# Optimization experiments

Measured on AMD Instinct MI355X. Metric: run time of the kernel, lower is better.

Reference implementation:

```python
import jax, jax.numpy as jnp
import numpy as np

N, F, E = 2048, 512, 32  # batch, n_features (attention length), embedding_dim


def setup_inputs() -> dict:
    key = jax.random.key(0)
    ks = jax.random.split(key, 8)
    xav = np.sqrt(2.0 / (F + E))  # xavier_normal std for [F, E] params
    X = jax.random.normal(ks[0], (N, F), dtype=jnp.float32)
    Xi = jax.random.randint(ks[1], (N,), 0, 2).astype(jnp.float32)
    idx = jax.random.randint(ks[2], (N,), 0, F)
    I = jax.nn.one_hot(idx, F, dtype=jnp.float32)  # one-hot feature selector
    S = (jax.random.uniform(ks[3], (N, F)) < 0.5).astype(jnp.float32)
    S = S.at[:, 0].set(1.0)  # guarantee non-empty context per row
    return {
        "X": X, "Xi": Xi, "I": I, "S": S,
        "xi_w": jax.random.normal(ks[4], (F, E), jnp.float32) * xav,
        "xi_b": jax.random.normal(ks[5], (F, E), jnp.float32) * xav,
        "xs_w": jax.random.normal(ks[6], (F, E), jnp.float32) * xav,
        "xs_b": jax.random.normal(ks[7], (F, E), jnp.float32) * xav,
    }


def stable_softmax(x):
    # softmax along last dim; rows that are entirely -inf produce zeros
    m = jnp.max(x, axis=-1, keepdims=True)
    m = jnp.where(jnp.isfinite(m), m, jnp.zeros_like(m))
    e = jnp.exp(x - m)
    s = jnp.sum(e, axis=-1, keepdims=True)
    return e / jnp.maximum(s, jnp.asarray(1e-9, x.dtype))


def reference(X, Xi, I, S, xi_w, xi_b, xs_w, xs_b):
    # --- map_xs (attention aggregator) ---
    # FX: [N, F, E]; note the original reuses xs_featurizer_bias for the I-term
    FX = X[:, :, None] * xs_w[None] + xs_b[None] + (I @ xs_b)[:, None, :]
    keep = (S[:, :, None] * S[:, None, :]) > 0  # [N, F, F]
    mask = jnp.where(keep, 0.0, -jnp.inf).astype(FX.dtype)
    scale = jnp.asarray(1.0 / np.sqrt(E), FX.dtype)
    scores = mask + jnp.einsum('nqe,nke->nqk', FX * scale, FX)
    attn = stable_softmax(scores)  # [N, F, F]
    Fxs = jnp.einsum('nqk,nke->nqe', attn, FX).sum(axis=1) / S.sum(axis=1)[:, None]  # [N, E]
    # --- map_xi ---
    Iw = I @ xi_w  # [N, E]
    Ib = I @ xi_b  # [N, E]
    Fxi = Xi[:, None] * Iw + Ib
    # --- score / logz / logprob (binary, exp score) ---
    ulogp = jnp.log(jnp.exp(jnp.sum(Fxi * Fxs, axis=-1)))
    s0 = jnp.exp(jnp.sum(Ib * Fxs, axis=-1))          # Xi = 0
    s1 = jnp.exp(jnp.sum((Iw + Ib) * Fxs, axis=-1))   # Xi = 1
    logz = jnp.log(s0 + s1)
    return ulogp - logz  # [N]
```

## Files before the change

kernel.cpp:

```cpp
#include <hip/hip_runtime.h>
#include <math.h>

#define FF 512
#define EE 32
#define RS 40
#define FCAP 416
#define NTCAP 26

typedef __attribute__((ext_vector_type(8))) short bf16x8;
typedef __attribute__((ext_vector_type(4))) float f32x4;

#define SFOLD 0.5050092f

__device__ __forceinline__ unsigned short f2bf(float x) {
    unsigned int u = __float_as_uint(x);
    return (unsigned short)((u + 0x7fffu + ((u >> 16) & 1u)) >> 16);
}

__device__ __forceinline__ void zh4(f32x4 d, float4 g, float& z, float& h) {
    float e0 = __builtin_amdgcn_exp2f(d[0]);
    float e1 = __builtin_amdgcn_exp2f(d[1]);
    float e2 = __builtin_amdgcn_exp2f(d[2]);
    float e3 = __builtin_amdgcn_exp2f(d[3]);
    z += (e0 + e1) + (e2 + e3);
    h = fmaf(e0, g.x, fmaf(e1, g.y, fmaf(e2, g.z, fmaf(e3, g.w, h))));
}

template <int NC>
__device__ __forceinline__ void fused_cols(const unsigned short* __restrict__ myrow,
                                           const float* __restrict__ gs,
                                           float* __restrict__ a_sh,
                                           int c0, int nt, int cnt, float pad,
                                           int lane, int grp) {
    bf16x8 bf[NC];
#pragma unroll
    for (int c = 0; c < NC; ++c)
        bf[c] = *(const bf16x8*)(myrow + (size_t)(c0 + c) * 16 * RS);
    float zA[NC], zB[NC], hA[NC], hB[NC];
#pragma unroll
    for (int c = 0; c < NC; ++c) { zA[c] = 0.f; zB[c] = 0.f; hA[c] = 0.f; hB[c] = 0.f; }
    const unsigned short* ap = myrow;
    const float* gp = gs + grp * 4;
    int i = 0;
    for (; i + 2 <= nt; i += 2) {
        bf16x8 a0 = *(const bf16x8*)(ap);
        bf16x8 a1 = *(const bf16x8*)(ap + 16 * RS);
        ap += 32 * RS;
        float4 g0 = *(const float4*)(gp);
        float4 g1 = *(const float4*)(gp + 16);
        gp += 32;
#pragma unroll
        for (int c = 0; c < NC; ++c) {
            f32x4 d0 = {0.f, 0.f, 0.f, 0.f};
            f32x4 d1 = {0.f, 0.f, 0.f, 0.f};
            d0 = __builtin_amdgcn_mfma_f32_16x16x32_bf16(a0, bf[c], d0, 0, 0, 0);
            d1 = __builtin_amdgcn_mfma_f32_16x16x32_bf16(a1, bf[c], d1, 0, 0, 0);
            zh4(d0, g0, zA[c], hA[c]);
            zh4(d1, g1, zB[c], hB[c]);
        }
    }
    if (i < nt) {
        bf16x8 a0 = *(const bf16x8*)(ap);
        float4 g0 = *(const float4*)(gp);
#pragma unroll
        for (int c = 0; c < NC; ++c) {
            f32x4 d0 = {0.f, 0.f, 0.f, 0.f};
            d0 = __builtin_amdgcn_mfma_f32_16x16x32_bf16(a0, bf[c], d0, 0, 0, 0);
            zh4(d0, g0, zA[c], hA[c]);
        }
    }
#pragma unroll
    for (int c = 0; c < NC; ++c) {
        float z = zA[c] + zB[c];
        float h = hA[c] + hB[c];
        z += __shfl_xor(z, 16); z += __shfl_xor(z, 32);
        h += __shfl_xor(h, 16); h += __shfl_xor(h, 32);
        int q = (c0 + c) * 16 + lane;
        float val = (lane < 16 && q < cnt) ? h / fmaxf(z - pad, 1e-9f) : 0.f;
        val += __shfl_xor(val, 1);
        val += __shfl_xor(val, 2);
        val += __shfl_xor(val, 4);
        val += __shfl_xor(val, 8);
        if (lane == 0) atomicAdd(a_sh, val);
    }
}

extern "C" __global__ void __launch_bounds__(512, 8)
model_kernel(const float* __restrict__ X, const float* __restrict__ Xi,
             const float* __restrict__ I, const float* __restrict__ S,
             const float* __restrict__ xi_w, const float* __restrict__ xi_b,
             const float* __restrict__ xs_w, const float* __restrict__ xs_b,
             float* __restrict__ out) {
    const int n = blockIdx.x;
    const int tid = threadIdx.x;
    const int lane = tid & 63;
    const int wv = tid >> 6;
    const int l15 = lane & 15;
    const int grp = lane >> 4;

    __shared__ __align__(16) unsigned short fxb[FCAP * RS];
    __shared__ unsigned short lst[FF];
    __shared__ __align__(16) float gs[FCAP];
    __shared__ __align__(16) float idxb[EE];
    __shared__ __align__(16) float iw_sh[EE];
    __shared__ float a_sh;
    __shared__ int sh_idx;
    __shared__ int wbase[8];

    const float* Srow = S + (size_t)n * FF;
    const float* Irow = I + (size_t)n * FF;
    const float* Xrow = X + (size_t)n * FF;

    if (Irow[tid] > 0.5f) sh_idx = tid;
    bool act = Srow[tid] > 0.f;
    unsigned long long m = __ballot(act);
    int nb = __popcll(m & ((1ull << lane) - 1ull));
    if (lane == 0) wbase[wv] = __popcll(m);
    __syncthreads();

    int off = 0;
    for (int i = 0; i < wv; ++i) off += wbase[i];
    if (act) lst[off + nb] = (unsigned short)tid;
    int cntr = 0;
#pragma unroll
    for (int i = 0; i < 8; ++i) cntr += wbase[i];
    const int cnt = (cntr < FCAP) ? cntr : FCAP;
    int nt0 = (cnt + 15) >> 4;
    const int nt = (nt0 < NTCAP) ? nt0 : NTCAP;
    const int ntp16 = nt * 16;
    const int jend = ((nt + 1) >> 1) * 32;
    const int idx = sh_idx;
    if (tid < EE) {
        idxb[tid] = xs_b[idx * EE + tid];
        iw_sh[tid] = xi_w[idx * EE + tid];
    }
    if (tid == 0) a_sh = 0.f;
    __syncthreads();

    for (int jb = 0; jb < jend; jb += 64) {
        int j = jb + (tid >> 3);
        int e4 = (tid & 7) * 4;
        float part = 0.f;
        if (j < jend) {
            unsigned short h0 = 0, h1 = 0, h2 = 0, h3 = 0;
            if (j < cnt) {
                int f = lst[j];
                float xv = Xrow[f];
                float4 w4 = *(const float4*)(xs_w + f * EE + e4);
                float4 b4 = *(const float4*)(xs_b + f * EE + e4);
                float4 i4 = *(const float4*)(idxb + e4);
                float r0 = SFOLD * fmaf(xv, w4.x, b4.x + i4.x);
                float r1 = SFOLD * fmaf(xv, w4.y, b4.y + i4.y);
                float r2 = SFOLD * fmaf(xv, w4.z, b4.z + i4.z);
                float r3 = SFOLD * fmaf(xv, w4.w, b4.w + i4.w);
                h0 = f2bf(r0); h1 = f2bf(r1); h2 = f2bf(r2); h3 = f2bf(r3);
                const float* iw = iw_sh + e4;
                part = fmaf(r0, iw[0], fmaf(r1, iw[1], fmaf(r2, iw[2], r3 * iw[3])));
            }
            ushort4 pk = make_ushort4(h0, h1, h2, h3);
            *(ushort4*)(fxb + j * RS + e4) = pk;
        }
        part += __shfl_xor(part, 1);
        part += __shfl_xor(part, 2);
        part += __shfl_xor(part, 4);
        if ((tid & 7) == 0 && j < jend) gs[j] = part;
    }
    __syncthreads();

    const unsigned short* myrow = fxb + (size_t)l15 * RS + grp * 8;
    const float pad = (float)(ntp16 - cnt);

    const int cbase = nt >> 3, crem = nt & 7;
    const int ncols = cbase + (wv < crem ? 1 : 0);
    const int c0 = wv * cbase + (wv < crem ? wv : crem);

    switch (ncols) {
        case 1: fused_cols<1>(myrow, gs, &a_sh, c0, nt, cnt, pad, lane, grp); break;
        case 2: fused_cols<2>(myrow, gs, &a_sh, c0, nt, cnt, pad, lane, grp); break;
        case 3: fused_cols<3>(myrow, gs, &a_sh, c0, nt, cnt, pad, lane, grp); break;
        case 4: fused_cols<2>(myrow, gs, &a_sh, c0, nt, cnt, pad, lane, grp);
                fused_cols<2>(myrow, gs, &a_sh, c0 + 2, nt, cnt, pad, lane, grp); break;
        default: break;
    }
    __syncthreads();

    if (tid == 0) {
        float a = a_sh / ((float)cnt * SFOLD);
        float xiv = Xi[n];
        float mm = fmaxf(a, 0.f);
        float sp = mm + logf(__expf(a - mm) + __expf(-mm));
        out[n] = xiv * a - sp;
    }
}

extern "C" void kernel_launch(void* const* d_in, const int* in_sizes, int n_in,
                              void* d_out, int out_size, void* d_ws, size_t ws_size,
                              hipStream_t stream) {
    const float* X    = (const float*)d_in[0];
    const float* Xi   = (const float*)d_in[1];
    const float* I    = (const float*)d_in[2];
    const float* S    = (const float*)d_in[3];
    const float* xi_w = (const float*)d_in[4];
    const float* xi_b = (const float*)d_in[5];
    const float* xs_w = (const float*)d_in[6];
    const float* xs_b = (const float*)d_in[7];
    float* out = (float*)d_out;
    const int N = in_sizes[1];
    hipLaunchKernelGGL(model_kernel, dim3(N), dim3(512), 0, stream,
                       X, Xi, I, S, xi_w, xi_b, xs_w, xs_b, out);
}
```

Measured before the change: 102.4 us.

## Split attention work across column groups and key halves with shared partial sums

Reorganizes the fused score/softmax loop so waves are arranged as 4 column groups times 2 key-range halves, each processing more query columns per loaded key tile. Partial softmax denominators and numerators are accumulated per query into shared arrays via atomics, then normalized and reduced in a final pass. This aims to increase A-operand reuse and balance work across waves, at the cost of shared atomics, an extra barrier, and losing dual independent accumulators.

```diff
diff --git a/kernel.cpp b/kernel.cpp
--- a/kernel.cpp
+++ b/kernel.cpp
@@ -27,22 +27,21 @@
 }
 
 template <int NC>
-__device__ __forceinline__ void fused_cols(const unsigned short* __restrict__ myrow,
-                                           const float* __restrict__ gs,
-                                           float* __restrict__ a_sh,
-                                           int c0, int nt, int cnt, float pad,
-                                           int lane, int grp) {
+__device__ __forceinline__ void fused(const unsigned short* __restrict__ myrow,
+                                      const float* __restrict__ gs,
+                                      float* __restrict__ Zp, float* __restrict__ Hp,
+                                      int c0, int s_lo, int s_hi, int lane, int grp) {
     bf16x8 bf[NC];
 #pragma unroll
     for (int c = 0; c < NC; ++c)
         bf[c] = *(const bf16x8*)(myrow + (size_t)(c0 + c) * 16 * RS);
-    float zA[NC], zB[NC], hA[NC], hB[NC];
-#pragma unroll
-    for (int c = 0; c < NC; ++c) { zA[c] = 0.f; zB[c] = 0.f; hA[c] = 0.f; hB[c] = 0.f; }
-    const unsigned short* ap = myrow;
-    const float* gp = gs + grp * 4;
-    int i = 0;
-    for (; i + 2 <= nt; i += 2) {
+    float z[NC], h[NC];
+#pragma unroll
+    for (int c = 0; c < NC; ++c) { z[c] = 0.f; h[c] = 0.f; }
+    const unsigned short* ap = myrow + (size_t)s_lo * 16 * RS;
+    const float* gp = gs + s_lo * 16 + grp * 4;
+    int s = s_lo;
+    for (; s + 2 <= s_hi; s += 2) {
         bf16x8 a0 = *(const bf16x8*)(ap);
         bf16x8 a1 = *(const bf16x8*)(ap + 16 * RS);
         ap += 32 * RS;
@@ -55,33 +54,29 @@
             f32x4 d1 = {0.f, 0.f, 0.f, 0.f};
             d0 = __builtin_amdgcn_mfma_f32_16x16x32_bf16(a0, bf[c], d0, 0, 0, 0);
             d1 = __builtin_amdgcn_mfma_f32_16x16x32_bf16(a1, bf[c], d1, 0, 0, 0);
-            zh4(d0, g0, zA[c], hA[c]);
-            zh4(d1, g1, zB[c], hB[c]);
-        }
-    }
-    if (i < nt) {
+            zh4(d0, g0, z[c], h[c]);
+            zh4(d1, g1, z[c], h[c]);
+        }
+    }
+    if (s < s_hi) {
         bf16x8 a0 = *(const bf16x8*)(ap);
         float4 g0 = *(const float4*)(gp);
 #pragma unroll
         for (int c = 0; c < NC; ++c) {
             f32x4 d0 = {0.f, 0.f, 0.f, 0.f};
             d0 = __builtin_amdgcn_mfma_f32_16x16x32_bf16(a0, bf[c], d0, 0, 0, 0);
-            zh4(d0, g0, zA[c], hA[c]);
+            zh4(d0, g0, z[c], h[c]);
         }
     }
 #pragma unroll
     for (int c = 0; c < NC; ++c) {
-        float z = zA[c] + zB[c];
-        float h = hA[c] + hB[c];
-        z += __shfl_xor(z, 16); z += __shfl_xor(z, 32);
-        h += __shfl_xor(h, 16); h += __shfl_xor(h, 32);
-        int q = (c0 + c) * 16 + lane;
-        float val = (lane < 16 && q < cnt) ? h / fmaxf(z - pad, 1e-9f) : 0.f;
-        val += __shfl_xor(val, 1);
-        val += __shfl_xor(val, 2);
-        val += __shfl_xor(val, 4);
-        val += __shfl_xor(val, 8);
-        if (lane == 0) atomicAdd(a_sh, val);
+        float zz = z[c], hh = h[c];
+        zz += __shfl_xor(zz, 16); zz += __shfl_xor(zz, 32);
+        hh += __shfl_xor(hh, 16); hh += __shfl_xor(hh, 32);
+        if (lane < 16) {
+            atomicAdd(&Zp[(c0 + c) * 16 + lane], zz);
+            atomicAdd(&Hp[(c0 + c) * 16 + lane], hh);
+        }
     }
 }
 
@@ -101,6 +96,8 @@
     __shared__ __align__(16) unsigned short fxb[FCAP * RS];
     __shared__ unsigned short lst[FF];
     __shared__ __align__(16) float gs[FCAP];
+    __shared__ __align__(16) float Zp[FCAP];
+    __shared__ __align__(16) float Hp[FCAP];
     __shared__ __align__(16) float idxb[EE];
     __shared__ __align__(16) float iw_sh[EE];
     __shared__ float a_sh;
@@ -112,6 +109,8 @@
     const float* Xrow = X + (size_t)n * FF;
 
     if (Irow[tid] > 0.5f) sh_idx = tid;
+    if (tid < FCAP) { Zp[tid] = 0.f; Hp[tid] = 0.f; }
+    if (tid == 0) a_sh = 0.f;
     bool act = Srow[tid] > 0.f;
     unsigned long long m = __ballot(act);
     int nb = __popcll(m & ((1ull << lane) - 1ull));
@@ -128,20 +127,18 @@
     int nt0 = (cnt + 15) >> 4;
     const int nt = (nt0 < NTCAP) ? nt0 : NTCAP;
     const int ntp16 = nt * 16;
-    const int jend = ((nt + 1) >> 1) * 32;
     const int idx = sh_idx;
     if (tid < EE) {
         idxb[tid] = xs_b[idx * EE + tid];
         iw_sh[tid] = xi_w[idx * EE + tid];
     }
-    if (tid == 0) a_sh = 0.f;
-    __syncthreads();
-
-    for (int jb = 0; jb < jend; jb += 64) {
+    __syncthreads();
+
+    for (int jb = 0; jb < ntp16; jb += 64) {
         int j = jb + (tid >> 3);
         int e4 = (tid & 7) * 4;
         float part = 0.f;
-        if (j < jend) {
+        if (j < ntp16) {
             unsigned short h0 = 0, h1 = 0, h2 = 0, h3 = 0;
             if (j < cnt) {
                 int f = lst[j];
@@ -163,24 +160,40 @@
         part += __shfl_xor(part, 1);
         part += __shfl_xor(part, 2);
         part += __shfl_xor(part, 4);
-        if ((tid & 7) == 0 && j < jend) gs[j] = part;
+        if ((tid & 7) == 0 && j < ntp16) gs[j] = part;
     }
     __syncthreads();
 
     const unsigned short* myrow = fxb + (size_t)l15 * RS + grp * 8;
     const float pad = (float)(ntp16 - cnt);
 
-    const int cbase = nt >> 3, crem = nt & 7;
-    const int ncols = cbase + (wv < crem ? 1 : 0);
-    const int c0 = wv * cbase + (wv < crem ? wv : crem);
-
-    switch (ncols) {
-        case 1: fused_cols<1>(myrow, gs, &a_sh, c0, nt, cnt, pad, lane, grp); break;
-        case 2: fused_cols<2>(myrow, gs, &a_sh, c0, nt, cnt, pad, lane, grp); break;
-        case 3: fused_cols<3>(myrow, gs, &a_sh, c0, nt, cnt, pad, lane, grp); break;
-        case 4: fused_cols<2>(myrow, gs, &a_sh, c0, nt, cnt, pad, lane, grp);
-                fused_cols<2>(myrow, gs, &a_sh, c0 + 2, nt, cnt, pad, lane, grp); break;
-        default: break;
+    const int cg = wv & 3;
+    const int ih = wv >> 2;
+    const int gbase = nt >> 2, grem = nt & 3;
+    const int ncols = gbase + (cg < grem ? 1 : 0);
+    int c0 = cg * gbase + (cg < grem ? cg : grem);
+    const int shalf = nt >> 1;
+    const int s_lo = ih ? shalf : 0;
+    const int s_hi = ih ? nt : shalf;
+
+    for (int done = 0; done < ncols; ) {
+        int nc = ncols - done;
+        if (nc >= 4)      { fused<4>(myrow, gs, Zp, Hp, c0 + done, s_lo, s_hi, lane, grp); done += 4; }
+        else if (nc == 3) { fused<3>(myrow, gs, Zp, Hp, c0 + done, s_lo, s_hi, lane, grp); done += 3; }
+        else if (nc == 2) { fused<2>(myrow, gs, Zp, Hp, c0 + done, s_lo, s_hi, lane, grp); done += 2; }
+        else              { fused<1>(myrow, gs, Zp, Hp, c0 + done, s_lo, s_hi, lane, grp); done += 1; }
+    }
+    __syncthreads();
+
+    {
+        float val = (tid < cnt) ? Hp[tid] / fmaxf(Zp[tid] - pad, 1e-9f) : 0.f;
+        val += __shfl_xor(val, 1);
+        val += __shfl_xor(val, 2);
+        val += __shfl_xor(val, 4);
+        val += __shfl_xor(val, 8);
+        val += __shfl_xor(val, 16);
+        val += __shfl_xor(val, 32);
+        if (lane == 0) atomicAdd(&a_sh, val);
     }
     __syncthreads();
 
```

After: 152.6 us. 49.1% more time.

## Build FX rows per thread directly, dropping the compaction index list and one barrier

Applied to the files above, without the earlier changes.

Each thread now loads its own feature's xs_w/xs_b rows and computes X*w+b before the ballot, so the global loads overlap the active-count prefix scan. After compaction it writes the full 32-wide bf16 row and the gs dot product straight to its compacted slot. This removes the lst indirection, the idxb/iw_sh shared staging, one __syncthreads and the shuffle reduction. The price is higher register pressure (32 floats per thread), per-thread strided row loads and a separate zero-padding loop. The ncols==3 case is also split into a 2-column plus a 1-column call, which cuts register pressure further.

```diff
diff --git a/kernel.cpp b/kernel.cpp
--- a/kernel.cpp
+++ b/kernel.cpp
@@ -99,28 +99,39 @@
     const int grp = lane >> 4;
 
     __shared__ __align__(16) unsigned short fxb[FCAP * RS];
-    __shared__ unsigned short lst[FF];
     __shared__ __align__(16) float gs[FCAP];
-    __shared__ __align__(16) float idxb[EE];
-    __shared__ __align__(16) float iw_sh[EE];
     __shared__ float a_sh;
     __shared__ int sh_idx;
     __shared__ int wbase[8];
 
     const float* Srow = S + (size_t)n * FF;
     const float* Irow = I + (size_t)n * FF;
-    const float* Xrow = X + (size_t)n * FF;
 
     if (Irow[tid] > 0.5f) sh_idx = tid;
+    if (tid == 0) a_sh = 0.f;
     bool act = Srow[tid] > 0.f;
-    unsigned long long m = __ballot(act);
-    int nb = __popcll(m & ((1ull << lane) - 1ull));
-    if (lane == 0) wbase[wv] = __popcll(m);
+    float xv = X[(size_t)n * FF + tid];
+    float4 rr[8];
+    if (act) {
+        const float* wp = xs_w + (size_t)tid * EE;
+        const float* bp = xs_b + (size_t)tid * EE;
+#pragma unroll
+        for (int m = 0; m < 8; ++m) {
+            float4 w4 = *(const float4*)(wp + m * 4);
+            float4 b4 = *(const float4*)(bp + m * 4);
+            rr[m].x = fmaf(xv, w4.x, b4.x);
+            rr[m].y = fmaf(xv, w4.y, b4.y);
+            rr[m].z = fmaf(xv, w4.z, b4.z);
+            rr[m].w = fmaf(xv, w4.w, b4.w);
+        }
+    }
+    unsigned long long mb = __ballot(act);
+    int nb = __popcll(mb & ((1ull << lane) - 1ull));
+    if (lane == 0) wbase[wv] = __popcll(mb);
     __syncthreads();
 
     int off = 0;
     for (int i = 0; i < wv; ++i) off += wbase[i];
-    if (act) lst[off + nb] = (unsigned short)tid;
     int cntr = 0;
 #pragma unroll
     for (int i = 0; i < 8; ++i) cntr += wbase[i];
@@ -130,40 +141,45 @@
     const int ntp16 = nt * 16;
     const int jend = ((nt + 1) >> 1) * 32;
     const int idx = sh_idx;
-    if (tid < EE) {
-        idxb[tid] = xs_b[idx * EE + tid];
-        iw_sh[tid] = xi_w[idx * EE + tid];
-    }
-    if (tid == 0) a_sh = 0.f;
-    __syncthreads();
-
-    for (int jb = 0; jb < jend; jb += 64) {
-        int j = jb + (tid >> 3);
-        int e4 = (tid & 7) * 4;
-        float part = 0.f;
-        if (j < jend) {
-            unsigned short h0 = 0, h1 = 0, h2 = 0, h3 = 0;
-            if (j < cnt) {
-                int f = lst[j];
-                float xv = Xrow[f];
-                float4 w4 = *(const float4*)(xs_w + f * EE + e4);
-                float4 b4 = *(const float4*)(xs_b + f * EE + e4);
-                float4 i4 = *(const float4*)(idxb + e4);
-                float r0 = SFOLD * fmaf(xv, w4.x, b4.x + i4.x);
-                float r1 = SFOLD * fmaf(xv, w4.y, b4.y + i4.y);
-                float r2 = SFOLD * fmaf(xv, w4.z, b4.z + i4.z);
-                float r3 = SFOLD * fmaf(xv, w4.w, b4.w + i4.w);
-                h0 = f2bf(r0); h1 = f2bf(r1); h2 = f2bf(r2); h3 = f2bf(r3);
-                const float* iw = iw_sh + e4;
-                part = fmaf(r0, iw[0], fmaf(r1, iw[1], fmaf(r2, iw[2], r3 * iw[3])));
+
+    if (act) {
+        int pos = off + nb;
+        if (pos < FCAP) {
+            const float* ib  = xs_b + (size_t)idx * EE;
+            const float* iwp = xi_w + (size_t)idx * EE;
+            float g = 0.f;
+#pragma unroll
+            for (int m = 0; m < 4; ++m) {
+                float4 iA = *(const float4*)(ib + m * 8);
+                float4 iB = *(const float4*)(ib + m * 8 + 4);
+                float4 wA = *(const float4*)(iwp + m * 8);
+                float4 wB = *(const float4*)(iwp + m * 8 + 4);
+                float r0 = SFOLD * (rr[2 * m].x + iA.x);
+                float r1 = SFOLD * (rr[2 * m].y + iA.y);
+                float r2 = SFOLD * (rr[2 * m].z + iA.z);
+                float r3 = SFOLD * (rr[2 * m].w + iA.w);
+                float r4 = SFOLD * (rr[2 * m + 1].x + iB.x);
+                float r5 = SFOLD * (rr[2 * m + 1].y + iB.y);
+                float r6 = SFOLD * (rr[2 * m + 1].z + iB.z);
+                float r7 = SFOLD * (rr[2 * m + 1].w + iB.w);
+                g = fmaf(r0, wA.x, fmaf(r1, wA.y, fmaf(r2, wA.z, fmaf(r3, wA.w, g))));
+                g = fmaf(r4, wB.x, fmaf(r5, wB.y, fmaf(r6, wB.z, fmaf(r7, wB.w, g))));
+                bf16x8 pk;
+                pk[0] = (short)f2bf(r0); pk[1] = (short)f2bf(r1);
+                pk[2] = (short)f2bf(r2); pk[3] = (short)f2bf(r3);
+                pk[4] = (short)f2bf(r4); pk[5] = (short)f2bf(r5);
+                pk[6] = (short)f2bf(r6); pk[7] = (short)f2bf(r7);
+                *(bf16x8*)(fxb + (size_t)pos * RS + m * 8) = pk;
             }
-            ushort4 pk = make_ushort4(h0, h1, h2, h3);
-            *(ushort4*)(fxb + j * RS + e4) = pk;
-        }
-        part += __shfl_xor(part, 1);
-        part += __shfl_xor(part, 2);
-        part += __shfl_xor(part, 4);
-        if ((tid & 7) == 0 && j < jend) gs[j] = part;
+            gs[pos] = g;
+        }
+    }
+    for (int j = cnt + tid; j < jend; j += 512) {
+        bf16x8 zk = {0, 0, 0, 0, 0, 0, 0, 0};
+#pragma unroll
+        for (int m = 0; m < 4; ++m)
+            *(bf16x8*)(fxb + (size_t)j * RS + m * 8) = zk;
+        gs[j] = 0.f;
     }
     __syncthreads();
 
@@ -177,7 +193,8 @@
     switch (ncols) {
         case 1: fused_cols<1>(myrow, gs, &a_sh, c0, nt, cnt, pad, lane, grp); break;
         case 2: fused_cols<2>(myrow, gs, &a_sh, c0, nt, cnt, pad, lane, grp); break;
-        case 3: fused_cols<3>(myrow, gs, &a_sh, c0, nt, cnt, pad, lane, grp); break;
+        case 3: fused_cols<2>(myrow, gs, &a_sh, c0, nt, cnt, pad, lane, grp);
+                fused_cols<1>(myrow, gs, &a_sh, c0 + 2, nt, cnt, pad, lane, grp); break;
         case 4: fused_cols<2>(myrow, gs, &a_sh, c0, nt, cnt, pad, lane, grp);
                 fused_cols<2>(myrow, gs, &a_sh, c0 + 2, nt, cnt, pad, lane, grp); break;
         default: break;
```

After: 106.3 us. 3.8% more time.
